# Kernel optimization log

Measured on AMD Instinct MI355X. Metric: run time of the kernel, lower is better.

The kernel has to match this reference:

```python
import jax, jax.numpy as jnp
import numpy as np

REPLACE = 4
REMAIN = 32
EPS = 1e-12


def _l2norm(x, axis):
    return x / jnp.maximum(jnp.linalg.norm(x, axis=axis, keepdims=True), EPS)


def setup_inputs() -> dict:
    key = jax.random.key(0)
    ks = jax.random.split(key, 16)
    B, d = 4096, 64
    n_users, n_entities, n_items = 100000, 200000, 50000
    K, n_cans, n_rel = 64, 64, 100
    return {
        "users": jax.random.randint(ks[0], (B,), 0, n_users),
        "items": jax.random.randint(ks[1], (B,), 0, n_items),
        "kg_neighbors": jax.random.randint(ks[2], (n_items, K), 0, n_entities),
        "all_candidates": jax.random.randint(ks[3], (n_rel, n_cans), 0, n_entities),
        "neighbor_relations": jax.random.randint(ks[4], (n_items, K), 0, n_rel),
        "user_all_embeddings": jax.random.normal(ks[5], (n_users, d), jnp.float32),
        "entity_all_embeddings": jax.random.normal(ks[6], (n_entities, d), jnp.float32),
        "item_embeddings": jax.random.normal(ks[7], (B, d), jnp.float32),
        "ui_W": jax.random.normal(ks[8], (2 * d, d), jnp.float32) / np.sqrt(2 * d),
        "ui_b": jnp.zeros((d,), jnp.float32),
        "e1_W": jax.random.normal(ks[9], (d, d), jnp.float32) / np.sqrt(d),
        "e1_b": jnp.zeros((d,), jnp.float32),
        "e2_W": jax.random.normal(ks[10], (d, d), jnp.float32) / np.sqrt(d),
        "e2_b": jnp.zeros((d,), jnp.float32),
    }


def reference(users, items, kg_neighbors, all_candidates, neighbor_relations,
              user_all_embeddings, entity_all_embeddings, item_embeddings,
              ui_W, ui_b, e1_W, e1_b, e2_W, e2_b):
    B = users.shape[0]
    d = user_all_embeddings.shape[1]
    idx_dtype = kg_neighbors.dtype

    neighbors = kg_neighbors[items]                      # [B, K]
    users_e = user_all_embeddings[users]                 # [B, d]
    ui_e = _l2norm(jnp.concatenate([users_e, item_embeddings], axis=1) @ ui_W + ui_b, 1)  # [B, d]

    # Step 1: score neighbors, pick top replace_num
    ne = _l2norm(entity_all_embeddings[neighbors] @ e1_W + e1_b, 2)   # [B, K, d]
    scores1 = jnp.einsum('bd,bkd->bk', ui_e, ne)
    logits1 = jax.nn.softmax(scores1, axis=1)
    step1_prob, step1_idx = jax.lax.top_k(logits1, REPLACE)          # [B, R]
    replaced = jnp.take_along_axis(neighbors, step1_idx, axis=1)     # [B, R]
    sel_rel = jnp.take_along_axis(neighbor_relations[items], step1_idx, axis=1)
    cf_kg1 = kg_neighbors.at[items[:, None], step1_idx].set(
        jnp.zeros((B, REPLACE), idx_dtype))
    ap1 = jnp.log(jnp.mean(step1_prob, axis=1))                      # [B]

    # Step 2: candidate pruning + sampling
    cands = all_candidates[sel_rel]                                  # [B, R, C]
    cands_e = entity_all_embeddings[cands]                           # [B, R, C, d]
    scores2 = jnp.einsum('bd,brcd->brc', users_e, cands_e)
    _, remain_idx = jax.lax.top_k(scores2, REMAIN)                   # [B, R, M]
    cands = jnp.take_along_axis(cands, remain_idx, axis=2).reshape(B * REPLACE, REMAIN)

    replaced_e = _l2norm(entity_all_embeddings[replaced] @ e1_W + e1_b, 2)
    replaced_e = replaced_e.reshape(B * REPLACE, d)
    cands_e2 = _l2norm(entity_all_embeddings[cands] @ e2_W + e2_b, 2)  # [BR, M, d]
    ui_rep = jnp.repeat(ui_e, REPLACE, axis=0)                         # [BR, d]
    s2 = jnp.einsum('nd,nmd->nm', ui_rep * replaced_e, cands_e2)       # [BR, M]
    logp2 = jax.nn.log_softmax(s2, axis=1)

    skey = jax.random.key(42)
    step2_idx = jax.random.categorical(skey, logp2, axis=1)           # [BR]
    rows = jnp.arange(B * REPLACE)
    step2_prob = jnp.exp(logp2[rows, step2_idx]).reshape(B, REPLACE)
    sel_ent = cands[rows, step2_idx].reshape(B, REPLACE)
    cf_kg2 = kg_neighbors.at[items[:, None], step1_idx].set(sel_ent.astype(idx_dtype))
    ap2 = jnp.log(jnp.mean(step1_prob, axis=1)) + jnp.log(jnp.mean(step2_prob, axis=1))
    return (cf_kg1, ap1, cf_kg2, ap2)
```

## Files before the change

### kernel.cpp

```cpp
#include <hip/hip_runtime.h>
#include <stdint.h>

#define EPS_NORM 1e-12f
#define F32_TINY 1.17549435e-38f

static __device__ __forceinline__ int rfl(int v) {
  return __builtin_amdgcn_readfirstlane(v);
}

__device__ __forceinline__ void threefry2x32(uint32_t k0, uint32_t k1,
                                             uint32_t x0, uint32_t x1,
                                             uint32_t& o0, uint32_t& o1) {
  uint32_t ks2 = k0 ^ k1 ^ 0x1BD11BDAu;
  x0 += k0; x1 += k1;
#define TF_ROT(r) { x0 += x1; x1 = (x1 << (r)) | (x1 >> (32 - (r))); x1 ^= x0; }
  TF_ROT(13) TF_ROT(15) TF_ROT(26) TF_ROT(6)
  x0 += k1; x1 += ks2 + 1u;
  TF_ROT(17) TF_ROT(29) TF_ROT(16) TF_ROT(24)
  x0 += ks2; x1 += k0 + 2u;
  TF_ROT(13) TF_ROT(15) TF_ROT(26) TF_ROT(6)
  x0 += k0; x1 += k1 + 3u;
  TF_ROT(17) TF_ROT(29) TF_ROT(16) TF_ROT(24)
  x0 += k1; x1 += ks2 + 4u;
  TF_ROT(13) TF_ROT(15) TF_ROT(26) TF_ROT(6)
  x0 += ks2; x1 += k0 + 5u;
#undef TF_ROT
  o0 = x0; o1 = x1;
}

#define PERM_IDX(p) ((((p) & 7) << 3) | ((p) >> 3))

__global__ __launch_bounds__(256) void k_phase1(
    const float* __restrict__ E, const int* __restrict__ allc,
    const float* __restrict__ W1, const float* __restrict__ b1,
    const float* __restrict__ W2, const float* __restrict__ b2,
    const float* __restrict__ U, const int* __restrict__ users,
    const float* __restrict__ Iemb, const float* __restrict__ uiW,
    const float* __restrict__ uib, const int* __restrict__ kg,
    float* __restrict__ T1, float* __restrict__ T2c,
    float* __restrict__ uiE, float* __restrict__ out0, float* __restrict__ out2) {
  __shared__ float SM[8192];
  const int blk = blockIdx.x, tid = threadIdx.x;
  const int wv = tid >> 6, lane = tid & 63;
  const int NT1B = 782, NT2B = 25, NUIB = 256;
  if (blk < NT1B + NT2B) {
    const bool isT1 = blk < NT1B;
    {
      const float* W = isT1 ? W1 : W2;
      for (int idx = tid; idx < 4096; idx += 256) {
        int k = idx >> 6, c = idx & 63;
        int cg = c & 7, ci = c >> 3;
        SM[k * 64 + ((ci >> 2) * 8 + cg) * 4 + (ci & 3)] = W[idx];
      }
    }
    __syncthreads();
    const int rg = lane >> 3, cg = lane & 7;
    const int sub = lane >> 5, r = lane & 31;
    const float* bias = isT1 ? b1 : b2;
    float bv[8];
#pragma unroll
    for (int ci = 0; ci < 8; ++ci) bv[ci] = bias[ci * 8 + cg];
    float* eTw = SM + 4096 + wv * 1024;
    const float4* eT4 = reinterpret_cast<const float4*>(eTw);
    const float4* W4 = reinterpret_cast<const float4*>(SM);
#pragma unroll 1
    for (int t = 0; t < 2; ++t) {
      int batch = (isT1 ? blk : blk - NT1B) * 2 + t;
      int rbase = batch * 128 + wv * 32;
      if (isT1 && rbase >= 200000) continue;
      int srow = isT1 ? (rbase + r) : allc[rbase + r];
      const float4* Er = reinterpret_cast<const float4*>(E + (size_t)srow * 64);
      float4 a0 = Er[sub * 4 + 0], a1 = Er[sub * 4 + 1];
      float4 a2 = Er[sub * 4 + 2], a3 = Er[sub * 4 + 3];
      float4 a4 = Er[8 + sub * 4 + 0], a5 = Er[8 + sub * 4 + 1];
      float4 a6 = Er[8 + sub * 4 + 2], a7 = Er[8 + sub * 4 + 3];
      float y[4][8];
#pragma unroll
      for (int ri = 0; ri < 4; ++ri)
#pragma unroll
        for (int ci = 0; ci < 8; ++ci) y[ri][ci] = 0.f;
      {
        float ev[16] = {a0.x, a0.y, a0.z, a0.w, a1.x, a1.y, a1.z, a1.w,
                        a2.x, a2.y, a2.z, a2.w, a3.x, a3.y, a3.z, a3.w};
#pragma unroll
        for (int kk = 0; kk < 16; ++kk)
          eTw[(sub * 16 + kk) * 32 + r] = ev[kk];
#pragma unroll 8
        for (int kk = 0; kk < 32; ++kk) {
          float4 e4 = eT4[kk * 8 + rg];
          float4 wa = W4[kk * 16 + cg];
          float4 wb = W4[kk * 16 + 8 + cg];
          float ev4[4] = {e4.x, e4.y, e4.z, e4.w};
          float wv8[8] = {wa.x, wa.y, wa.z, wa.w, wb.x, wb.y, wb.z, wb.w};
#pragma unroll
          for (int ri = 0; ri < 4; ++ri)
#pragma unroll
            for (int ci = 0; ci < 8; ++ci)
              y[ri][ci] = fmaf(ev4[ri], wv8[ci], y[ri][ci]);
        }
      }
      {
        float ev[16] = {a4.x, a4.y, a4.z, a4.w, a5.x, a5.y, a5.z, a5.w,
                        a6.x, a6.y, a6.z, a6.w, a7.x, a7.y, a7.z, a7.w};
#pragma unroll
        for (int kk = 0; kk < 16; ++kk)
          eTw[(sub * 16 + kk) * 32 + r] = ev[kk];
#pragma unroll 8
        for (int kk = 0; kk < 32; ++kk) {
          float4 e4 = eT4[kk * 8 + rg];
          float4 wa = W4[(32 + kk) * 16 + cg];
          float4 wb = W4[(32 + kk) * 16 + 8 + cg];
          float ev4[4] = {e4.x, e4.y, e4.z, e4.w};
          float wv8[8] = {wa.x, wa.y, wa.z, wa.w, wb.x, wb.y, wb.z, wb.w};
#pragma unroll
          for (int ri = 0; ri < 4; ++ri)
#pragma unroll
            for (int ci = 0; ci < 8; ++ci)
              y[ri][ci] = fmaf(ev4[ri], wv8[ci], y[ri][ci]);
        }
      }
#pragma unroll
      for (int ri = 0; ri < 4; ++ri)
#pragma unroll
        for (int ci = 0; ci < 8; ++ci)
          y[ri][ci] = __fadd_rn(y[ri][ci], bv[ci]);
#pragma unroll
      for (int ri = 0; ri < 4; ++ri) {
        float A0 = __fadd_rn(__fmul_rn(y[ri][0], y[ri][0]),
                             __fmul_rn(y[ri][4], y[ri][4]));
        float A1 = __fadd_rn(__fmul_rn(y[ri][1], y[ri][1]),
                             __fmul_rn(y[ri][5], y[ri][5]));
        float A2 = __fadd_rn(__fmul_rn(y[ri][2], y[ri][2]),
                             __fmul_rn(y[ri][6], y[ri][6]));
        float A3 = __fadd_rn(__fmul_rn(y[ri][3], y[ri][3]),
                             __fmul_rn(y[ri][7], y[ri][7]));
        float B0 = __fadd_rn(A0, A2), B1 = __fadd_rn(A1, A3);
        float C = __fadd_rn(B0, B1);
        C = __fadd_rn(C, __shfl_xor(C, 4));
        C = __fadd_rn(C, __shfl_xor(C, 2));
        C = __fadd_rn(C, __shfl_xor(C, 1));
        float denom = fmaxf(sqrtf(C), EPS_NORM);
        int row = rbase + rg * 4 + ri;
        if (isT1) {
          float4* drow = reinterpret_cast<float4*>(T1 + (size_t)row * 64 + cg * 8);
          drow[0] = make_float4(y[ri][0] / denom, y[ri][1] / denom,
                                y[ri][2] / denom, y[ri][3] / denom);
          drow[1] = make_float4(y[ri][4] / denom, y[ri][5] / denom,
                                y[ri][6] / denom, y[ri][7] / denom);
        } else {
          float* drow = T2c + (size_t)row * 64;
#pragma unroll
          for (int ci = 0; ci < 8; ++ci) drow[ci * 8 + cg] = y[ri][ci] / denom;
        }
      }
    }
  } else if (blk < NT1B + NT2B + NUIB) {
    int ub = blk - (NT1B + NT2B);
    for (int i = tid; i < 8192; i += 256) SM[i] = uiW[i];
    __syncthreads();
    float bl = uib[lane];
#pragma unroll 1
    for (int t = 0; t < 4; ++t) {
      int b = ub * 16 + wv * 4 + t;
      int usr = rfl(users[b]);
      const float* ur = U + (size_t)usr * 64;
      const float* ir = Iemb + (size_t)b * 64;
      float y = 0.f;
#pragma unroll
      for (int k = 0; k < 64; ++k) y = fmaf(ur[k], SM[k * 64 + lane], y);
#pragma unroll
      for (int k = 0; k < 64; ++k) y = fmaf(ir[k], SM[(64 + k) * 64 + lane], y);
      y += bl;
      float ss = y * y;
#pragma unroll
      for (int off = 32; off; off >>= 1) ss += __shfl_xor(ss, off);
      float yn = y / fmaxf(sqrtf(ss), EPS_NORM);
      uiE[(size_t)b * 64 + lane] = yn;
    }
  } else {
    const int4* kg4 = reinterpret_cast<const int4*>(kg);
    float4* o4 = reinterpret_cast<float4*>(out0);
    float4* o24 = reinterpret_cast<float4*>(out2);
    for (int i = (blk - 1063) * 256 + tid; i < 800000; i += 200 * 256) {
      int4 v = kg4[i];
      float4 f = make_float4((float)v.x, (float)v.y, (float)v.z, (float)v.w);
      o4[i] = f;
      o24[i] = f;
    }
  }
}

__global__ __launch_bounds__(256) void k_init(const int* __restrict__ kg,
                                              float* __restrict__ out0,
                                              int* __restrict__ wkg2, int n) {
  int i = blockIdx.x * 256 + threadIdx.x;
  if (i < n) { int v = kg[i]; out0[i] = (float)v; wkg2[i] = v; }
}

__device__ __forceinline__ void transform_row(const float4* __restrict__ Er,
                                              const float* __restrict__ W,
                                              const float* __restrict__ bias,
                                              float (&yn)[64]) {
  float y[64];
#pragma unroll
  for (int j = 0; j < 64; ++j) y[j] = 0.f;
  float4 c0 = Er[0], c1 = Er[1], c2 = Er[2], c3 = Er[3];
#pragma unroll 1
  for (int cc = 0; cc < 4; ++cc) {
    float4 n0, n1, n2, n3;
    if (cc < 3) { n0 = Er[cc * 4 + 4]; n1 = Er[cc * 4 + 5];
                  n2 = Er[cc * 4 + 6]; n3 = Er[cc * 4 + 7]; }
    float ev[16] = {c0.x, c0.y, c0.z, c0.w, c1.x, c1.y, c1.z, c1.w,
                    c2.x, c2.y, c2.z, c2.w, c3.x, c3.y, c3.z, c3.w};
#pragma unroll
    for (int k2i = 0; k2i < 16; ++k2i) {
      const float4* Wr = reinterpret_cast<const float4*>(
          W + ((size_t)(cc * 16 + k2i)) * 64);
      float ek = ev[k2i];
#pragma unroll
      for (int j4 = 0; j4 < 16; ++j4) {
        float4 w = Wr[j4];
        y[j4 * 4 + 0] = fmaf(ek, w.x, y[j4 * 4 + 0]);
        y[j4 * 4 + 1] = fmaf(ek, w.y, y[j4 * 4 + 1]);
        y[j4 * 4 + 2] = fmaf(ek, w.z, y[j4 * 4 + 2]);
        y[j4 * 4 + 3] = fmaf(ek, w.w, y[j4 * 4 + 3]);
      }
    }
    c0 = n0; c1 = n1; c2 = n2; c3 = n3;
  }
  const float4* B4 = reinterpret_cast<const float4*>(bias);
#pragma unroll
  for (int j4 = 0; j4 < 16; ++j4) {
    float4 bb = B4[j4];
    float bv[4] = {bb.x, bb.y, bb.z, bb.w};
#pragma unroll
    for (int t = 0; t < 4; ++t) y[j4 * 4 + t] = __fadd_rn(y[j4 * 4 + t], bv[t]);
  }
  float S1[32];
#pragma unroll
  for (int i = 0; i < 32; ++i)
    S1[i] = __fadd_rn(__fmul_rn(y[i], y[i]), __fmul_rn(y[i + 32], y[i + 32]));
#pragma unroll
  for (int i = 0; i < 16; ++i) S1[i] = __fadd_rn(S1[i], S1[i + 16]);
#pragma unroll
  for (int i = 0; i < 8; ++i)  S1[i] = __fadd_rn(S1[i], S1[i + 8]);
#pragma unroll
  for (int i = 0; i < 4; ++i)  S1[i] = __fadd_rn(S1[i], S1[i + 4]);
#pragma unroll
  for (int i = 0; i < 2; ++i)  S1[i] = __fadd_rn(S1[i], S1[i + 2]);
  float ss = __fadd_rn(S1[0], S1[1]);
  float denom = fmaxf(sqrtf(ss), EPS_NORM);
#pragma unroll
  for (int j = 0; j < 64; ++j) yn[j] = y[j] / denom;
}

__global__ __launch_bounds__(256) void k_transform64(
    const float* __restrict__ src, const int* __restrict__ gidx,
    const float* __restrict__ W, const float* __restrict__ bias,
    float* __restrict__ out, int nrows) {
  __shared__ float Wl[4096];
  for (int i = threadIdx.x; i < 4096; i += 256) Wl[i] = W[i];
  __syncthreads();
  int wid = threadIdx.x >> 6, lane = threadIdx.x & 63;
  int row = rfl(blockIdx.x * 4 + wid);
  if (row >= nrows) return;
  int srow = rfl(gidx ? gidx[row] : row);
  const float* er = src + (size_t)srow * 64;
  float y = 0.f;
#pragma unroll
  for (int k = 0; k < 64; ++k) y = fmaf(er[k], Wl[k * 64 + lane], y);
  y += bias[lane];
  float ss = y * y;
#pragma unroll
  for (int off = 32; off; off >>= 1) ss += __shfl_xor(ss, off);
  float yn = y / fmaxf(sqrtf(ss), EPS_NORM);
  out[(size_t)row * 64 + lane] = yn;
}

__global__ __launch_bounds__(256) void k_ui(
    const float* __restrict__ U, const int* __restrict__ users,
    const float* __restrict__ Iemb, const float* __restrict__ W,
    const float* __restrict__ bias, float* __restrict__ out, int B) {
  __shared__ float Wl[8192];
  for (int i = threadIdx.x; i < 8192; i += 256) Wl[i] = W[i];
  __syncthreads();
  int wid = threadIdx.x >> 6, lane = threadIdx.x & 63;
  int b = rfl(blockIdx.x * 4 + wid);
  if (b >= B) return;
  int usr = rfl(users[b]);
  const float* ur = U + (size_t)usr * 64;
  const float* ir = Iemb + (size_t)b * 64;
  float y = 0.f;
#pragma unroll
  for (int k = 0; k < 64; ++k) y = fmaf(ur[k], Wl[k * 64 + lane], y);
#pragma unroll
  for (int k = 0; k < 64; ++k) y = fmaf(ir[k], Wl[(64 + k) * 64 + lane], y);
  y += bias[lane];
  float ss = y * y;
#pragma unroll
  for (int off = 32; off; off >>= 1) ss += __shfl_xor(ss, off);
  float yn = y / fmaxf(sqrtf(ss), EPS_NORM);
  out[(size_t)b * 64 + lane] = yn;
}

__device__ __forceinline__ void score1_tail(
    float s, int lane, int b, int item, int nb,
    const int* __restrict__ nrel,
    float* __restrict__ out0, float* __restrict__ ap1_out,
    int* __restrict__ s1_idx, int* __restrict__ s1_rel, int* __restrict__ s1_ent,
    float* __restrict__ lmp1, int* __restrict__ wkg2) {
  float m = s;
#pragma unroll
  for (int off = 32; off; off >>= 1) m = fmaxf(m, __shfl_xor(m, off));
  float ex = expf(s - m);
  float sum = ex;
#pragma unroll
  for (int off = 32; off; off >>= 1) sum += __shfl_xor(sum, off);
  float p = ex / sum;
  int rank = 0;
  for (int k2 = 0; k2 < 64; ++k2) {
    float pv = __shfl(p, k2);
    rank += (pv > p || (pv == p && k2 < lane)) ? 1 : 0;
  }
  float acc = 0.f;
#pragma unroll
  for (int rr = 0; rr < 4; ++rr) {
    unsigned long long msk = __ballot(rank == rr);
    int src = __ffsll(msk) - 1;
    acc += __shfl(p, src);
  }
  float lm = logf(acc * 0.25f);
  if (lane == 0) { ap1_out[b] = lm; lmp1[b] = lm; }
  if (rank < 4) {
    s1_idx[b * 4 + rank] = lane;
    s1_ent[b * 4 + rank] = nb;
    s1_rel[b * 4 + rank] = nrel[(size_t)item * 64 + lane];
    out0[(size_t)item * 64 + lane] = 0.0f;
    wkg2[(size_t)item * 64 + lane] = 0;
  }
}

__global__ __launch_bounds__(256) void k_score1g(
    const int* __restrict__ items, const int* __restrict__ kg,
    const int* __restrict__ nrel, const float* __restrict__ T1,
    const float* __restrict__ uiE,
    float* __restrict__ out0, float* __restrict__ ap1_out,
    int* __restrict__ s1_idx, int* __restrict__ s1_rel, int* __restrict__ s1_ent,
    float* __restrict__ lmp1, int* __restrict__ wkg2) {
  int tid = threadIdx.x, wv = tid >> 6, lane = tid & 63;
  int b = rfl(blockIdx.x * 4 + wv);
  int item = rfl(items[b]);
  int nb = kg[(size_t)item * 64 + lane];
  const float4* R = reinterpret_cast<const float4*>(T1 + (size_t)nb * 64);
  float yn[64];
#pragma unroll
  for (int p4 = 0; p4 < 16; ++p4) {
    float4 v = R[p4];
    yn[PERM_IDX(4 * p4 + 0)] = v.x;
    yn[PERM_IDX(4 * p4 + 1)] = v.y;
    yn[PERM_IDX(4 * p4 + 2)] = v.z;
    yn[PERM_IDX(4 * p4 + 3)] = v.w;
  }
  const float4* Ur = reinterpret_cast<const float4*>(uiE + (size_t)b * 64);
  float D[32];
#pragma unroll
  for (int i4 = 0; i4 < 8; ++i4) {
    float4 ua = Ur[i4], ub = Ur[i4 + 8];
    float uav[4] = {ua.x, ua.y, ua.z, ua.w};
    float ubv[4] = {ub.x, ub.y, ub.z, ub.w};
#pragma unroll
    for (int t = 0; t < 4; ++t) {
      int i = i4 * 4 + t;
      D[i] = __fadd_rn(__fmul_rn(yn[i], uav[t]), __fmul_rn(yn[i + 32], ubv[t]));
    }
  }
#pragma unroll
  for (int i = 0; i < 16; ++i) D[i] = __fadd_rn(D[i], D[i + 16]);
#pragma unroll
  for (int i = 0; i < 8; ++i)  D[i] = __fadd_rn(D[i], D[i + 8]);
#pragma unroll
  for (int i = 0; i < 4; ++i)  D[i] = __fadd_rn(D[i], D[i + 4]);
#pragma unroll
  for (int i = 0; i < 2; ++i)  D[i] = __fadd_rn(D[i], D[i + 2]);
  float s = __fadd_rn(D[0], D[1]);
  score1_tail(s, lane, b, item, nb, nrel, out0, ap1_out, s1_idx, s1_rel, s1_ent,
              lmp1, wkg2);
}

__global__ __launch_bounds__(256) void k_score1(
    const int* __restrict__ items, const int* __restrict__ kg,
    const int* __restrict__ nrel, const float* __restrict__ E,
    const float* __restrict__ W1, const float* __restrict__ b1,
    const float* __restrict__ uiE,
    float* __restrict__ out0, float* __restrict__ ap1_out,
    int* __restrict__ s1_idx, int* __restrict__ s1_rel, int* __restrict__ s1_ent,
    float* __restrict__ lmp1, int* __restrict__ wkg2) {
  int tid = threadIdx.x, wv = tid >> 6, lane = tid & 63;
  int b = rfl(blockIdx.x * 4 + wv);
  int item = rfl(items[b]);
  int nb = kg[(size_t)item * 64 + lane];
  const float4* Er = reinterpret_cast<const float4*>(E + (size_t)nb * 64);
  float yn[64];
  transform_row(Er, W1, b1, yn);
  const float4* Ur = reinterpret_cast<const float4*>(uiE + (size_t)b * 64);
  float D[32];
#pragma unroll
  for (int i4 = 0; i4 < 8; ++i4) {
    float4 ua = Ur[i4], ub = Ur[i4 + 8];
    float uav[4] = {ua.x, ua.y, ua.z, ua.w};
    float ubv[4] = {ub.x, ub.y, ub.z, ub.w};
#pragma unroll
    for (int t = 0; t < 4; ++t) {
      int i = i4 * 4 + t;
      D[i] = __fadd_rn(__fmul_rn(yn[i], uav[t]), __fmul_rn(yn[i + 32], ubv[t]));
    }
  }
#pragma unroll
  for (int i = 0; i < 16; ++i) D[i] = __fadd_rn(D[i], D[i + 16]);
#pragma unroll
  for (int i = 0; i < 8; ++i)  D[i] = __fadd_rn(D[i], D[i + 8]);
#pragma unroll
  for (int i = 0; i < 4; ++i)  D[i] = __fadd_rn(D[i], D[i + 4]);
#pragma unroll
  for (int i = 0; i < 2; ++i)  D[i] = __fadd_rn(D[i], D[i + 2]);
  float s = __fadd_rn(D[0], D[1]);
  score1_tail(s, lane, b, item, nb, nrel, out0, ap1_out, s1_idx, s1_rel, s1_ent,
              lmp1, wkg2);
}

__global__ __launch_bounds__(256) void k_score2(
    const int* __restrict__ users, const int* __restrict__ s1_rel,
    const float* __restrict__ U, const float* __restrict__ E,
    const int* __restrict__ allc, int* __restrict__ kept, int N) {
  int wid = threadIdx.x >> 6, lane = threadIdx.x & 63;
  int n = rfl(blockIdx.x * 4 + wid);
  if (n >= N) return;
  int b = n >> 2;
  int rel = rfl(s1_rel[n]);
  int usr = rfl(users[b]);
  int ent = allc[rel * 64 + lane];
  const float* ur = U + (size_t)usr * 64;
  const float4* e4 = reinterpret_cast<const float4*>(E + (size_t)ent * 64);
  float s = 0.f;
#pragma unroll
  for (int j4 = 0; j4 < 16; ++j4) {
    float4 t = e4[j4];
    s = fmaf(ur[4 * j4 + 0], t.x, s);
    s = fmaf(ur[4 * j4 + 1], t.y, s);
    s = fmaf(ur[4 * j4 + 2], t.z, s);
    s = fmaf(ur[4 * j4 + 3], t.w, s);
  }
  int rank = 0;
  for (int k2 = 0; k2 < 64; ++k2) {
    float sv = __shfl(s, k2);
    rank += (sv > s || (sv == s && k2 < lane)) ? 1 : 0;
  }
  if (rank < 32) kept[n * 32 + rank] = (lane << 18) | ent;
}

template <bool PERMQ>
__device__ __forceinline__ void sample_body(
    float q, int n, int b, int lane,
    const int* __restrict__ items, const int* __restrict__ s1_idx,
    int rel, const float* __restrict__ T2c, const int* __restrict__ kept,
    float* __restrict__ p2, int* __restrict__ wkg2) {
  int m = lane & 31;
  int pk = kept[n * 32 + m];
  int c = pk >> 18;
  int ent = pk & 0x3FFFF;
  const float4* c4 = reinterpret_cast<const float4*>(T2c + ((size_t)rel * 64 + c) * 64);
  float s = 0.f;
#pragma unroll
  for (int j4 = 0; j4 < 16; ++j4) {
    float4 t = c4[j4];
    s = fmaf(__shfl(q, PERMQ ? PERM_IDX(4 * j4 + 0) : (4 * j4 + 0)), t.x, s);
    s = fmaf(__shfl(q, PERMQ ? PERM_IDX(4 * j4 + 1) : (4 * j4 + 1)), t.y, s);
    s = fmaf(__shfl(q, PERMQ ? PERM_IDX(4 * j4 + 2) : (4 * j4 + 2)), t.z, s);
    s = fmaf(__shfl(q, PERMQ ? PERM_IDX(4 * j4 + 3) : (4 * j4 + 3)), t.w, s);
  }
  float mx = s;
#pragma unroll
  for (int off = 1; off < 32; off <<= 1) mx = fmaxf(mx, __shfl_xor(mx, off));
  float shv = s - mx;
  float se = expf(shv);
  float sum = se;
#pragma unroll
  for (int off = 1; off < 32; off <<= 1) sum += __shfl_xor(sum, off);
  float logp = shv - logf(sum);
  uint32_t h0, h1;
  threefry2x32(0u, 42u, 0u, (uint32_t)(n * 32 + m), h0, h1);
  uint32_t bits = h0 ^ h1;
  float u0 = __uint_as_float((bits >> 9) | 0x3F800000u) - 1.0f;
  float uu = fmaxf(u0, F32_TINY);
  float g = -logf(-logf(uu));
  float z = g + logp;
  float bz = z; int bm = m;
#pragma unroll
  for (int off = 1; off < 32; off <<= 1) {
    float oz = __shfl_xor(bz, off);
    int om = __shfl_xor(bm, off);
    if (oz > bz || (oz == bz && om < bm)) { bz = oz; bm = om; }
  }
  if (lane == bm) {
    p2[n] = expf(logp);
    int col = s1_idx[n];
    int item = items[b];
    atomicMax(&wkg2[(size_t)item * 64 + col], ((b + 1) << 18) | ent);
  }
}

__global__ __launch_bounds__(256) void k_sample2(
    const int* __restrict__ items,
    const int* __restrict__ s1_idx, const int* __restrict__ s1_rel,
    const int* __restrict__ s1_ent, const float* __restrict__ T1,
    const float* __restrict__ T2c, const float* __restrict__ uiE,
    const int* __restrict__ kept,
    float* __restrict__ p2, int* __restrict__ wkg2, int N) {
  int tid = threadIdx.x, wid = tid >> 6, lane = tid & 63;
  int n = rfl(blockIdx.x * 4 + wid);
  if (n >= N) return;
  int b = n >> 2;
  int rel = rfl(s1_rel[n]);
  int repl = rfl(s1_ent[n]);
  int pl = PERM_IDX(lane);
  float q = uiE[(size_t)b * 64 + pl] * T1[(size_t)repl * 64 + lane];
  sample_body<true>(q, n, b, lane, items, s1_idx, rel, T2c, kept, p2, wkg2);
}

__global__ __launch_bounds__(256) void k_sample(
    const int* __restrict__ items,
    const int* __restrict__ s1_idx, const int* __restrict__ s1_rel,
    const int* __restrict__ s1_ent,
    const float* __restrict__ E, const float* __restrict__ W1,
    const float* __restrict__ b1, const float* __restrict__ T2c,
    const float* __restrict__ uiE, const int* __restrict__ kept,
    float* __restrict__ p2, int* __restrict__ wkg2, int N) {
  __shared__ float Wl[4096];
  int tid = threadIdx.x;
  for (int i = tid; i < 4096; i += 256) Wl[i] = W1[i];
  __syncthreads();
  int wid = tid >> 6, lane = tid & 63;
  int n = rfl(blockIdx.x * 4 + wid);
  if (n >= N) return;
  int b = n >> 2;
  int rel = rfl(s1_rel[n]);
  int repl = rfl(s1_ent[n]);
  const float* er = E + (size_t)repl * 64;
  float y = 0.f;
#pragma unroll
  for (int k2 = 0; k2 < 64; ++k2) y = fmaf(er[k2], Wl[k2 * 64 + lane], y);
  y += b1[lane];
  float ss = y * y;
#pragma unroll
  for (int off = 32; off; off >>= 1) ss += __shfl_xor(ss, off);
  float yn = y / fmaxf(sqrtf(ss), EPS_NORM);
  float q = uiE[(size_t)b * 64 + lane] * yn;
  sample_body<false>(q, n, b, lane, items, s1_idx, rel, T2c, kept, p2, wkg2);
}

__global__ __launch_bounds__(256) void k_fin2(
    const int* __restrict__ items, const int* __restrict__ s1_idx,
    const int* __restrict__ wkg2, const float* __restrict__ p2,
    const float* __restrict__ lmp1,
    float* __restrict__ out2, float* __restrict__ out3, int N, int B) {
  int i = blockIdx.x * 256 + threadIdx.x;
  if (i < N) {
    int b = i >> 2;
    int item = items[b];
    int col = s1_idx[i];
    int v = wkg2[(size_t)item * 64 + col];
    out2[(size_t)item * 64 + col] = (float)(v & 0x3FFFF);
  }
  if (i < B) {
    float a = ((p2[i * 4] + p2[i * 4 + 1]) + p2[i * 4 + 2]) + p2[i * 4 + 3];
    out3[i] = lmp1[i] + logf(a * 0.25f);
  }
}

__global__ __launch_bounds__(256) void k_fin(const int* __restrict__ wkg2,
                                             const float* __restrict__ p2,
                                             const float* __restrict__ lmp1,
                                             float* __restrict__ out2,
                                             float* __restrict__ out3,
                                             int n, int B) {
  int i = blockIdx.x * 256 + threadIdx.x;
  if (i < n) out2[i] = (float)(wkg2[i] & 0x3FFFF);
  if (i < B) {
    float a = ((p2[i * 4] + p2[i * 4 + 1]) + p2[i * 4 + 2]) + p2[i * 4 + 3];
    out3[i] = lmp1[i] + logf(a * 0.25f);
  }
}

extern "C" void kernel_launch(void* const* d_in, const int* in_sizes, int n_in,
                              void* d_out, int out_size, void* d_ws, size_t ws_size,
                              hipStream_t stream) {
  const int*   users = (const int*)d_in[0];
  const int*   items = (const int*)d_in[1];
  const int*   kg    = (const int*)d_in[2];
  const int*   allc  = (const int*)d_in[3];
  const int*   nrel  = (const int*)d_in[4];
  const float* U     = (const float*)d_in[5];
  const float* E     = (const float*)d_in[6];
  const float* Iemb  = (const float*)d_in[7];
  const float* uiW   = (const float*)d_in[8];
  const float* uib   = (const float*)d_in[9];
  const float* e1W   = (const float*)d_in[10];
  const float* e1b   = (const float*)d_in[11];
  const float* e2W   = (const float*)d_in[12];
  const float* e2b   = (const float*)d_in[13];

  const int B = 4096, NCELL = 3200000, NCAND = 6400, NR4 = 16384, NENT = 200000;

  float* out0    = (float*)d_out;
  float* out_ap1 = out0 + NCELL;
  float* out2    = out_ap1 + B;
  float* out_ap2 = out2 + NCELL;

  float* T2c  = (float*)d_ws;
  float* uiE  = T2c + 409600;
  int*   wkg2 = (int*)(uiE + 262144);
  int*   s1i  = wkg2 + NCELL;
  int*   s1r  = s1i + NR4;
  int*   s1e  = s1r + NR4;
  int*   kept = s1e + NR4;
  float* p2   = (float*)(kept + 524288);
  float* lmp1 = p2 + NR4;
  float* T1   = lmp1 + B;
  const size_t WS_NEED = ((size_t)(T1 + (size_t)NENT * 64) - (size_t)d_ws);
  const bool pathA = ws_size >= WS_NEED;

  if (pathA) {
    k_phase1<<<1263, 256, 0, stream>>>(E, allc, e1W, e1b, e2W, e2b, U, users,
                                       Iemb, uiW, uib, kg, T1, T2c, uiE,
                                       out0, out2);
    k_score1g<<<B / 4, 256, 0, stream>>>(items, kg, nrel, T1, uiE,
                                         out0, out_ap1, s1i, s1r, s1e, lmp1, wkg2);
    k_score2<<<(NR4 + 3) / 4, 256, 0, stream>>>(users, s1r, U, E, allc, kept, NR4);
    k_sample2<<<(NR4 + 3) / 4, 256, 0, stream>>>(items, s1i, s1r, s1e, T1, T2c,
                                                 uiE, kept, p2, wkg2, NR4);
    k_fin2<<<(NR4 + 255) / 256, 256, 0, stream>>>(items, s1i, wkg2, p2, lmp1,
                                                  out2, out_ap2, NR4, B);
  } else {
    k_init<<<(NCELL + 255) / 256, 256, 0, stream>>>(kg, out0, wkg2, NCELL);
    k_ui<<<(B + 3) / 4, 256, 0, stream>>>(U, users, Iemb, uiW, uib, uiE, B);
    k_transform64<<<(NCAND + 3) / 4, 256, 0, stream>>>(E, allc, e2W, e2b, T2c, NCAND);
    k_score1<<<B / 4, 256, 0, stream>>>(items, kg, nrel, E, e1W, e1b, uiE,
                                        out0, out_ap1, s1i, s1r, s1e, lmp1, wkg2);
    k_score2<<<(NR4 + 3) / 4, 256, 0, stream>>>(users, s1r, U, E, allc, kept, NR4);
    k_sample<<<(NR4 + 3) / 4, 256, 0, stream>>>(items, s1i, s1r, s1e, E, e1W, e1b,
                                                T2c, uiE, kept, p2, wkg2, NR4);
    k_fin<<<(NCELL + 255) / 256, 256, 0, stream>>>(wkg2, p2, lmp1, out2, out_ap2,
                                                   NCELL, B);
  }
}
```

Measured before the change: 135.9 us.

## Fuse step-1 scoring, candidate top-k and sampling into one per-batch kernel

Replaces the three kernels k_score1g, k_score2 and k_sample2 with a single k_step kernel that uses one block per batch row. Wave 0 does step-1 scoring and top-4 selection into shared memory, then all four waves run the candidate scoring, top-32 selection and Gumbel sampling for one replacement each. Zeroing of wkg2 moves into the phase1 copy loop. This removes two launches and the global round-trips for s1_rel, s1_ent and kept. In exchange, three waves sit idle during step 1 and phase1 now writes the whole wkg2 buffer.

Measured after the change: 135.5 us. About the same (-0.3%).

```diff
diff --git a/kernel.cpp b/kernel.cpp
--- a/kernel.cpp
+++ b/kernel.cpp
@@ -38,7 +38,8 @@
     const float* __restrict__ Iemb, const float* __restrict__ uiW,
     const float* __restrict__ uib, const int* __restrict__ kg,
     float* __restrict__ T1, float* __restrict__ T2c,
-    float* __restrict__ uiE, float* __restrict__ out0, float* __restrict__ out2) {
+    float* __restrict__ uiE, float* __restrict__ out0, float* __restrict__ out2,
+    int* __restrict__ wkg2) {
   __shared__ float SM[8192];
   const int blk = blockIdx.x, tid = threadIdx.x;
   const int wv = tid >> 6, lane = tid & 63;
@@ -181,12 +182,185 @@
     const int4* kg4 = reinterpret_cast<const int4*>(kg);
     float4* o4 = reinterpret_cast<float4*>(out0);
     float4* o24 = reinterpret_cast<float4*>(out2);
+    int4* wz = reinterpret_cast<int4*>(wkg2);
+    int4 z; z.x = 0; z.y = 0; z.z = 0; z.w = 0;
     for (int i = (blk - 1063) * 256 + tid; i < 800000; i += 200 * 256) {
       int4 v = kg4[i];
       float4 f = make_float4((float)v.x, (float)v.y, (float)v.z, (float)v.w);
       o4[i] = f;
       o24[i] = f;
-    }
+      wz[i] = z;
+    }
+  }
+}
+
+__global__ __launch_bounds__(256) void k_step(
+    const int* __restrict__ items, const int* __restrict__ users,
+    const int* __restrict__ kg, const int* __restrict__ nrel,
+    const int* __restrict__ allc, const float* __restrict__ E,
+    const float* __restrict__ T1, const float* __restrict__ T2c,
+    const float* __restrict__ uiE, const float* __restrict__ U,
+    float* __restrict__ out0, float* __restrict__ ap1_out,
+    int* __restrict__ s1i_g, float* __restrict__ lmp1,
+    float* __restrict__ p2, int* __restrict__ wkg2) {
+  __shared__ int s1_idx_sh[4], s1_rel_sh[4], s1_ent_sh[4];
+  __shared__ int kept_sh[128];
+  const int tid = threadIdx.x, wv = tid >> 6, lane = tid & 63;
+  const int b = blockIdx.x;
+  const int item = rfl(items[b]);
+  if (wv == 0) {
+    int nb = kg[(size_t)item * 64 + lane];
+    const float4* R = reinterpret_cast<const float4*>(T1 + (size_t)nb * 64);
+    float yn[64];
+#pragma unroll
+    for (int p4 = 0; p4 < 16; ++p4) {
+      float4 v = R[p4];
+      yn[PERM_IDX(4 * p4 + 0)] = v.x;
+      yn[PERM_IDX(4 * p4 + 1)] = v.y;
+      yn[PERM_IDX(4 * p4 + 2)] = v.z;
+      yn[PERM_IDX(4 * p4 + 3)] = v.w;
+    }
+    const float4* Ur = reinterpret_cast<const float4*>(uiE + (size_t)b * 64);
+    float D[32];
+#pragma unroll
+    for (int i4 = 0; i4 < 8; ++i4) {
+      float4 ua = Ur[i4], ub = Ur[i4 + 8];
+      float uav[4] = {ua.x, ua.y, ua.z, ua.w};
+      float ubv[4] = {ub.x, ub.y, ub.z, ub.w};
+#pragma unroll
+      for (int t = 0; t < 4; ++t) {
+        int i = i4 * 4 + t;
+        D[i] = __fadd_rn(__fmul_rn(yn[i], uav[t]), __fmul_rn(yn[i + 32], ubv[t]));
+      }
+    }
+#pragma unroll
+    for (int i = 0; i < 16; ++i) D[i] = __fadd_rn(D[i], D[i + 16]);
+#pragma unroll
+    for (int i = 0; i < 8; ++i)  D[i] = __fadd_rn(D[i], D[i + 8]);
+#pragma unroll
+    for (int i = 0; i < 4; ++i)  D[i] = __fadd_rn(D[i], D[i + 4]);
+#pragma unroll
+    for (int i = 0; i < 2; ++i)  D[i] = __fadd_rn(D[i], D[i + 2]);
+    float s = __fadd_rn(D[0], D[1]);
+    float m = s;
+#pragma unroll
+    for (int off = 32; off; off >>= 1) m = fmaxf(m, __shfl_xor(m, off));
+    float ex = expf(s - m);
+    float sum = ex;
+#pragma unroll
+    for (int off = 32; off; off >>= 1) sum += __shfl_xor(sum, off);
+    float p = ex / sum;
+    int rank = 0;
+    for (int k2 = 0; k2 < 64; ++k2) {
+      float pv = __shfl(p, k2);
+      rank += (pv > p || (pv == p && k2 < lane)) ? 1 : 0;
+    }
+    float acc = 0.f;
+#pragma unroll
+    for (int rr = 0; rr < 4; ++rr) {
+      unsigned long long msk = __ballot(rank == rr);
+      int src = __ffsll(msk) - 1;
+      acc += __shfl(p, src);
+    }
+    float lm = logf(acc * 0.25f);
+    if (lane == 0) { ap1_out[b] = lm; lmp1[b] = lm; }
+    if (rank < 4) {
+      s1_idx_sh[rank] = lane;
+      s1_ent_sh[rank] = nb;
+      s1_rel_sh[rank] = nrel[(size_t)item * 64 + lane];
+      s1i_g[b * 4 + rank] = lane;
+      out0[(size_t)item * 64 + lane] = 0.0f;
+    }
+  }
+  __syncthreads();
+  const int n = b * 4 + wv;
+  const int rel = rfl(s1_rel_sh[wv]);
+  const int repl = rfl(s1_ent_sh[wv]);
+  const int colsel = rfl(s1_idx_sh[wv]);
+  {
+    int usr = rfl(users[b]);
+    int ent = allc[rel * 64 + lane];
+    const float* ur = U + (size_t)usr * 64;
+    const float4* e4 = reinterpret_cast<const float4*>(E + (size_t)ent * 64);
+    float s = 0.f;
+#pragma unroll
+    for (int j4 = 0; j4 < 16; ++j4) {
+      float4 t = e4[j4];
+      s = fmaf(ur[4 * j4 + 0], t.x, s);
+      s = fmaf(ur[4 * j4 + 1], t.y, s);
+      s = fmaf(ur[4 * j4 + 2], t.z, s);
+      s = fmaf(ur[4 * j4 + 3], t.w, s);
+    }
+    int rank = 0;
+    for (int k2 = 0; k2 < 64; ++k2) {
+      float sv = __shfl(s, k2);
+      rank += (sv > s || (sv == s && k2 < lane)) ? 1 : 0;
+    }
+    if (rank < 32) kept_sh[wv * 32 + rank] = (lane << 18) | ent;
+  }
+  {
+    int m = lane & 31;
+    int pk = kept_sh[wv * 32 + m];
+    int c = pk >> 18;
+    int ent = pk & 0x3FFFF;
+    float q = uiE[(size_t)b * 64 + PERM_IDX(lane)] * T1[(size_t)repl * 64 + lane];
+    const float4* c4 = reinterpret_cast<const float4*>(
+        T2c + ((size_t)rel * 64 + c) * 64);
+    float s = 0.f;
+#pragma unroll
+    for (int j4 = 0; j4 < 16; ++j4) {
+      float4 t = c4[j4];
+      s = fmaf(__shfl(q, PERM_IDX(4 * j4 + 0)), t.x, s);
+      s = fmaf(__shfl(q, PERM_IDX(4 * j4 + 1)), t.y, s);
+      s = fmaf(__shfl(q, PERM_IDX(4 * j4 + 2)), t.z, s);
+      s = fmaf(__shfl(q, PERM_IDX(4 * j4 + 3)), t.w, s);
+    }
+    float mx = s;
+#pragma unroll
+    for (int off = 1; off < 32; off <<= 1) mx = fmaxf(mx, __shfl_xor(mx, off));
+    float shv = s - mx;
+    float se = expf(shv);
+    float sum = se;
+#pragma unroll
+    for (int off = 1; off < 32; off <<= 1) sum += __shfl_xor(sum, off);
+    float logp = shv - logf(sum);
+    uint32_t h0, h1;
+    threefry2x32(0u, 42u, 0u, (uint32_t)(n * 32 + m), h0, h1);
+    uint32_t bits = h0 ^ h1;
+    float u0 = __uint_as_float((bits >> 9) | 0x3F800000u) - 1.0f;
+    float uu = fmaxf(u0, F32_TINY);
+    float g = -logf(-logf(uu));
+    float z = g + logp;
+    float bz = z; int bm = m;
+#pragma unroll
+    for (int off = 1; off < 32; off <<= 1) {
+      float oz = __shfl_xor(bz, off);
+      int om = __shfl_xor(bm, off);
+      if (oz > bz || (oz == bz && om < bm)) { bz = oz; bm = om; }
+    }
+    if (lane == bm) {
+      p2[n] = expf(logp);
+      atomicMax(&wkg2[(size_t)item * 64 + colsel], ((b + 1) << 18) | ent);
+    }
+  }
+}
+
+__global__ __launch_bounds__(256) void k_fin2(
+    const int* __restrict__ items, const int* __restrict__ s1_idx,
+    const int* __restrict__ wkg2, const float* __restrict__ p2,
+    const float* __restrict__ lmp1,
+    float* __restrict__ out2, float* __restrict__ out3, int N, int B) {
+  int i = blockIdx.x * 256 + threadIdx.x;
+  if (i < N) {
+    int b = i >> 2;
+    int item = items[b];
+    int col = s1_idx[i];
+    int v = wkg2[(size_t)item * 64 + col];
+    out2[(size_t)item * 64 + col] = (float)(v & 0x3FFFF);
+  }
+  if (i < B) {
+    float a = ((p2[i * 4] + p2[i * 4 + 1]) + p2[i * 4 + 2]) + p2[i * 4 + 3];
+    out3[i] = lmp1[i] + logf(a * 0.25f);
   }
 }
 
@@ -338,53 +512,6 @@
     out0[(size_t)item * 64 + lane] = 0.0f;
     wkg2[(size_t)item * 64 + lane] = 0;
   }
-}
-
-__global__ __launch_bounds__(256) void k_score1g(
-    const int* __restrict__ items, const int* __restrict__ kg,
-    const int* __restrict__ nrel, const float* __restrict__ T1,
-    const float* __restrict__ uiE,
-    float* __restrict__ out0, float* __restrict__ ap1_out,
-    int* __restrict__ s1_idx, int* __restrict__ s1_rel, int* __restrict__ s1_ent,
-    float* __restrict__ lmp1, int* __restrict__ wkg2) {
-  int tid = threadIdx.x, wv = tid >> 6, lane = tid & 63;
-  int b = rfl(blockIdx.x * 4 + wv);
-  int item = rfl(items[b]);
-  int nb = kg[(size_t)item * 64 + lane];
-  const float4* R = reinterpret_cast<const float4*>(T1 + (size_t)nb * 64);
-  float yn[64];
-#pragma unroll
-  for (int p4 = 0; p4 < 16; ++p4) {
-    float4 v = R[p4];
-    yn[PERM_IDX(4 * p4 + 0)] = v.x;
-    yn[PERM_IDX(4 * p4 + 1)] = v.y;
-    yn[PERM_IDX(4 * p4 + 2)] = v.z;
-    yn[PERM_IDX(4 * p4 + 3)] = v.w;
-  }
-  const float4* Ur = reinterpret_cast<const float4*>(uiE + (size_t)b * 64);
-  float D[32];
-#pragma unroll
-  for (int i4 = 0; i4 < 8; ++i4) {
-    float4 ua = Ur[i4], ub = Ur[i4 + 8];
-    float uav[4] = {ua.x, ua.y, ua.z, ua.w};
-    float ubv[4] = {ub.x, ub.y, ub.z, ub.w};
-#pragma unroll
-    for (int t = 0; t < 4; ++t) {
-      int i = i4 * 4 + t;
-      D[i] = __fadd_rn(__fmul_rn(yn[i], uav[t]), __fmul_rn(yn[i + 32], ubv[t]));
-    }
-  }
-#pragma unroll
-  for (int i = 0; i < 16; ++i) D[i] = __fadd_rn(D[i], D[i + 16]);
-#pragma unroll
-  for (int i = 0; i < 8; ++i)  D[i] = __fadd_rn(D[i], D[i + 8]);
-#pragma unroll
-  for (int i = 0; i < 4; ++i)  D[i] = __fadd_rn(D[i], D[i + 4]);
-#pragma unroll
-  for (int i = 0; i < 2; ++i)  D[i] = __fadd_rn(D[i], D[i + 2]);
-  float s = __fadd_rn(D[0], D[1]);
-  score1_tail(s, lane, b, item, nb, nrel, out0, ap1_out, s1_idx, s1_rel, s1_ent,
-              lmp1, wkg2);
 }
 
 __global__ __launch_bounds__(256) void k_score1(
@@ -507,24 +634,6 @@
     int item = items[b];
     atomicMax(&wkg2[(size_t)item * 64 + col], ((b + 1) << 18) | ent);
   }
-}
-
-__global__ __launch_bounds__(256) void k_sample2(
-    const int* __restrict__ items,
-    const int* __restrict__ s1_idx, const int* __restrict__ s1_rel,
-    const int* __restrict__ s1_ent, const float* __restrict__ T1,
-    const float* __restrict__ T2c, const float* __restrict__ uiE,
-    const int* __restrict__ kept,
-    float* __restrict__ p2, int* __restrict__ wkg2, int N) {
-  int tid = threadIdx.x, wid = tid >> 6, lane = tid & 63;
-  int n = rfl(blockIdx.x * 4 + wid);
-  if (n >= N) return;
-  int b = n >> 2;
-  int rel = rfl(s1_rel[n]);
-  int repl = rfl(s1_ent[n]);
-  int pl = PERM_IDX(lane);
-  float q = uiE[(size_t)b * 64 + pl] * T1[(size_t)repl * 64 + lane];
-  sample_body<true>(q, n, b, lane, items, s1_idx, rel, T2c, kept, p2, wkg2);
 }
 
 __global__ __launch_bounds__(256) void k_sample(
@@ -558,25 +667,6 @@
   sample_body<false>(q, n, b, lane, items, s1_idx, rel, T2c, kept, p2, wkg2);
 }
 
-__global__ __launch_bounds__(256) void k_fin2(
-    const int* __restrict__ items, const int* __restrict__ s1_idx,
-    const int* __restrict__ wkg2, const float* __restrict__ p2,
-    const float* __restrict__ lmp1,
-    float* __restrict__ out2, float* __restrict__ out3, int N, int B) {
-  int i = blockIdx.x * 256 + threadIdx.x;
-  if (i < N) {
-    int b = i >> 2;
-    int item = items[b];
-    int col = s1_idx[i];
-    int v = wkg2[(size_t)item * 64 + col];
-    out2[(size_t)item * 64 + col] = (float)(v & 0x3FFFF);
-  }
-  if (i < B) {
-    float a = ((p2[i * 4] + p2[i * 4 + 1]) + p2[i * 4 + 2]) + p2[i * 4 + 3];
-    out3[i] = lmp1[i] + logf(a * 0.25f);
-  }
-}
-
 __global__ __launch_bounds__(256) void k_fin(const int* __restrict__ wkg2,
                                              const float* __restrict__ p2,
                                              const float* __restrict__ lmp1,
@@ -632,12 +722,9 @@
   if (pathA) {
     k_phase1<<<1263, 256, 0, stream>>>(E, allc, e1W, e1b, e2W, e2b, U, users,
                                        Iemb, uiW, uib, kg, T1, T2c, uiE,
-                                       out0, out2);
-    k_score1g<<<B / 4, 256, 0, stream>>>(items, kg, nrel, T1, uiE,
-                                         out0, out_ap1, s1i, s1r, s1e, lmp1, wkg2);
-    k_score2<<<(NR4 + 3) / 4, 256, 0, stream>>>(users, s1r, U, E, allc, kept, NR4);
-    k_sample2<<<(NR4 + 3) / 4, 256, 0, stream>>>(items, s1i, s1r, s1e, T1, T2c,
-                                                 uiE, kept, p2, wkg2, NR4);
+                                       out0, out2, wkg2);
+    k_step<<<B, 256, 0, stream>>>(items, users, kg, nrel, allc, E, T1, T2c,
+                                  uiE, U, out0, out_ap1, s1i, lmp1, p2, wkg2);
     k_fin2<<<(NR4 + 255) / 256, 256, 0, stream>>>(items, s1i, wkg2, p2, lmp1,
                                                   out2, out_ap2, NR4, B);
   } else {
```
